# Performance work log

Hardware: AMD Instinct MI355X
Metric: run time of the kernel (lower is better)

The kernel has to match this reference:

```python
import jax, jax.numpy as jnp
import numpy as np

B, DIN, DH, DOUT = 4096, 512, 1024, 256
DFF = 4 * DH
STEPS = 30
REF_DIM = 64
GAMMA = 0.5 * min(1.0, float(np.sqrt(REF_DIM / DIN)))  # dimension-scaled gamma
LN_EPS = 1e-5


def setup_inputs() -> dict:
    key = jax.random.key(0)
    ks = jax.random.split(key, 6)
    rn = lambda k, shp, s: (jax.random.normal(k, shp, jnp.float32) * s)
    return {
        "x": rn(ks[0], (B, DIN), 1.0),
        "embed_w": rn(ks[1], (DH, DIN), 0.02),
        "embed_b": jnp.zeros((DH,), jnp.float32),
        "W1": rn(ks[2], (DFF, DH), 0.02),
        "b1": jnp.zeros((DFF,), jnp.float32),
        "W2": rn(ks[3], (DH, DFF), 0.02),
        "b2": jnp.zeros((DH,), jnp.float32),
        "ln_g": jnp.ones((DH,), jnp.float32),
        "ln_b": jnp.zeros((DH,), jnp.float32),
        "head_w": rn(ks[4], (DOUT, DH), 0.02),
        "head_b": jnp.zeros((DOUT,), jnp.float32),
    }


def _spectral_normalize(W, n_iter=15):
    # power iteration (u, v treated as constants, like torch spectral_norm buffers)
    v0 = jnp.full((W.shape[1],), 1.0 / np.sqrt(W.shape[1]), W.dtype)
    def body(i, uv):
        _, v = uv
        u = W @ v
        u = u / (jnp.linalg.norm(u) + 1e-12)
        v = W.T @ u
        v = v / (jnp.linalg.norm(v) + 1e-12)
        return (u, v)
    u0 = W @ v0
    u0 = u0 / (jnp.linalg.norm(u0) + 1e-12)
    u, v = jax.lax.fori_loop(0, n_iter, body, (u0, v0))
    u = jax.lax.stop_gradient(u)
    v = jax.lax.stop_gradient(v)
    sigma = u @ (W @ v)  # grad flows through W here, as in torch
    return W / sigma


def _layernorm(h, g, b):
    mu = jnp.mean(h, axis=-1, keepdims=True)
    var = jnp.var(h, axis=-1, keepdims=True)
    return (h - mu) * jax.lax.rsqrt(var + LN_EPS) * g + b


def reference(x, embed_w, embed_b, W1, b1, W2, b2, ln_g, ln_b, head_w, head_b):
    W1n = _spectral_normalize(W1)
    W2n = _spectral_normalize(W2)
    x_emb = x @ embed_w.T + embed_b  # [B, DH]; constant across steps

    def ffn(h):
        hn = _layernorm(h, ln_g, ln_b)
        hid = jnp.tanh(hn @ W1n.T + b1)  # dropout p=0 -> identity
        return hid @ W2n.T + b2

    def step(h, _):
        h_target = ffn(h) + x_emb
        h_next = (1.0 - GAMMA) * h + GAMMA * h_target
        return h_next, None

    h, _ = jax.lax.scan(step, x_emb, None, length=STEPS)
    return h @ head_w.T + head_b
```

## Files before the change

kernel.cpp:

```cpp
#include <hip/hip_runtime.h>
#include <hip/hip_bf16.h>
#include <math.h>

#define B_    4096
#define DIN_  512
#define DH_   1024
#define DOUT_ 256
#define DFF_  4096
#define STEPS_ 30
#define GAMMA_ 0.17677669529663687f
#define LN_EPS_ 1e-5f

typedef __attribute__((ext_vector_type(8))) short short8;
typedef __attribute__((ext_vector_type(4))) float f32x4;

__device__ inline void gload_lds16(const void* g, void* l) {
  __builtin_amdgcn_global_load_lds(
      (const __attribute__((address_space(1))) unsigned int*)g,
      (__attribute__((address_space(3))) unsigned int*)l, 16, 0, 0);
}

__device__ inline float fast_tanh(float v) {
  const float e = __expf(2.f * v);
  return 1.f - 2.f * __builtin_amdgcn_rcpf(e + 1.f);
}

__device__ inline float bf2f(unsigned short u) {
  return __uint_as_float((unsigned)u << 16);
}

__global__ __launch_bounds__(512, 2) void gemm256(
    const __hip_bfloat16* __restrict__ A, const __hip_bfloat16* __restrict__ Bm,
    int M, int N, int K, int kc, int nt, const float* __restrict__ bias,
    int epi, __hip_bfloat16* __restrict__ bf16out) {
  __shared__ __align__(16) char lds[4][32768];
  const int tid = threadIdx.x;
  const int lane = tid & 63;
  const int wid = tid >> 6;
  const int wr = wid >> 2;
  const int wc = wid & 3;

  const int gx = gridDim.x;
  const int nwg = gx * gridDim.y;
  const int wg = blockIdx.y * gx + blockIdx.x;
  const int cpx = nwg >> 3;
  const int swz = (wg & 7) * cpx + (wg >> 3);
  const int bx = swz % gx, by = swz / gx;
  const int m0 = by * 256, n0 = bx * 256;
  const int zk = blockIdx.z * kc;

  const int srow = wid * 16 + (lane >> 2);
  const int scol = (lane & 3) * 8;

  f32x4 acc[8][4];
  const f32x4 zero = {0.f, 0.f, 0.f, 0.f};
#pragma unroll
  for (int i = 0; i < 8; ++i)
#pragma unroll
    for (int j = 0; j < 4; ++j) acc[i][j] = zero;

  auto STAGE = [&](int t) {
    const int kt = zk + t * 32;
    char* base = &lds[t & 3][0];
#pragma unroll
    for (int q = 0; q < 4; ++q) {
      const __hip_bfloat16* src =
          (q < 2) ? A + (size_t)(m0 + q * 128 + srow) * K + kt + scol
                  : Bm + (size_t)(n0 + (q - 2) * 128 + srow) * K + kt + scol;
      gload_lds16((const void*)src, (void*)(base + q * 8192 + wid * 1024));
    }
  };

  STAGE(0);
  STAGE(1);
  STAGE(2);

  const int ar = lane & 15;
  const int hb = (lane >> 4) * 16;

  for (int t = 0; t < nt; ++t) {
    const char* base = &lds[t & 3][0];
    if (t + 3 <= nt) {
      asm volatile("s_waitcnt vmcnt(8)" ::: "memory");
    } else if (t + 2 == nt) {
      asm volatile("s_waitcnt vmcnt(4)" ::: "memory");
    } else {
      asm volatile("s_waitcnt vmcnt(0)" ::: "memory");
    }
    __builtin_amdgcn_s_barrier();
    __builtin_amdgcn_sched_barrier(0);

    short8 av[8], bv[4];
#pragma unroll
    for (int mf = 0; mf < 8; ++mf)
      av[mf] = *(const short8*)(base + (wr * 128 + mf * 16 + ar) * 64 + hb);
#pragma unroll
    for (int nf = 0; nf < 4; ++nf)
      bv[nf] = *(const short8*)(base + 16384 + (wc * 64 + nf * 16 + ar) * 64 + hb);

    if (t + 3 < nt) STAGE(t + 3);

    asm volatile("s_waitcnt lgkmcnt(0)" ::: "memory");
    __builtin_amdgcn_sched_barrier(0);
    __builtin_amdgcn_s_setprio(1);
#pragma unroll
    for (int mf = 0; mf < 8; ++mf)
#pragma unroll
      for (int nf = 0; nf < 4; ++nf)
        acc[mf][nf] = __builtin_amdgcn_mfma_f32_16x16x32_bf16(av[mf], bv[nf], acc[mf][nf], 0, 0, 0);
    __builtin_amdgcn_s_setprio(0);
    __builtin_amdgcn_sched_barrier(0);
  }

  if (epi == 4) bf16out += (size_t)blockIdx.z * ((size_t)M * N);
  const int rb = (lane >> 4) * 4;
#pragma unroll
  for (int mf = 0; mf < 8; ++mf) {
#pragma unroll
    for (int nf = 0; nf < 4; ++nf) {
      const int col = n0 + wc * 64 + nf * 16 + ar;
      const float bvs = bias ? bias[col] : 0.f;
#pragma unroll
      for (int j = 0; j < 4; ++j) {
        const int row = m0 + wr * 128 + mf * 16 + rb + j;
        float v = acc[mf][nf][j] + bvs;
        if (epi == 1) v = fast_tanh(v);
        bf16out[(size_t)row * N + col] = __float2bfloat16(v);
      }
    }
  }
}

__global__ __launch_bounds__(256) void gemm_bt(
    const __hip_bfloat16* __restrict__ A, const __hip_bfloat16* __restrict__ Bm,
    int M, int N, int K, const float* __restrict__ bias, int epi,
    float* __restrict__ f32out, float* __restrict__ f32out2) {
  __shared__ __align__(16) short As[128 * 32];
  __shared__ __align__(16) short Bs[128 * 32];
  const int tid = threadIdx.x;
  const int lane = tid & 63;
  const int wid = tid >> 6;
  const int wr = wid >> 1, wc = wid & 1;

  const int gx = gridDim.x;
  const int nwg = gx * gridDim.y;
  const int wg = blockIdx.y * gx + blockIdx.x;
  const int cpx = nwg >> 3;
  const int swz = (wg & 7) * cpx + (wg >> 3);
  const int bx = swz % gx, by = swz / gx;

  const int m0 = by * 128, n0 = bx * 128;
  const int ldsrow = lane >> 2;
  const int col8 = (lane & 3) * 8;

  f32x4 acc[4][4];
  const f32x4 zero = {0.f, 0.f, 0.f, 0.f};
#pragma unroll
  for (int i = 0; i < 4; ++i)
#pragma unroll
    for (int j = 0; j < 4; ++j) acc[i][j] = zero;

  for (int kt = 0; kt < K; kt += 32) {
#pragma unroll
    for (int i = 0; i < 2; ++i) {
      const int seg = wid * 2 + i;
      gload_lds16(A + (size_t)(m0 + seg * 16 + ldsrow) * K + kt + col8,
                  (void*)(As + seg * 512));
      gload_lds16(Bm + (size_t)(n0 + seg * 16 + ldsrow) * K + kt + col8,
                  (void*)(Bs + seg * 512));
    }
    __syncthreads();
    short8 a[4], b[4];
#pragma unroll
    for (int mf = 0; mf < 4; ++mf)
      a[mf] = *(const short8*)&As[(wr * 64 + mf * 16 + (lane & 15)) * 32 + (lane >> 4) * 8];
#pragma unroll
    for (int nf = 0; nf < 4; ++nf)
      b[nf] = *(const short8*)&Bs[(wc * 64 + nf * 16 + (lane & 15)) * 32 + (lane >> 4) * 8];
#pragma unroll
    for (int mf = 0; mf < 4; ++mf)
#pragma unroll
      for (int nf = 0; nf < 4; ++nf)
        acc[mf][nf] = __builtin_amdgcn_mfma_f32_16x16x32_bf16(a[mf], b[nf], acc[mf][nf], 0, 0, 0);
    __syncthreads();
  }

  const int rbase = (lane >> 4) * 4;
  const int cin = lane & 15;
#pragma unroll
  for (int mf = 0; mf < 4; ++mf) {
#pragma unroll
    for (int nf = 0; nf < 4; ++nf) {
      const int col = n0 + wc * 64 + nf * 16 + cin;
      const float bv = bias[col];
#pragma unroll
      for (int j = 0; j < 4; ++j) {
        const int row = m0 + wr * 64 + mf * 16 + rbase + j;
        const float v = acc[mf][nf][j] + bv;
        const size_t idx = (size_t)row * N + col;
        if (epi == 0) {
          f32out[idx] = v;
          f32out2[idx] = v;
        } else {
          f32out[idx] = v;
        }
      }
    }
  }
}

__global__ __launch_bounds__(256) void reduce_ln_kernel(
    const __hip_bfloat16* __restrict__ ps, const float* __restrict__ b2,
    const float* __restrict__ xe, float* __restrict__ h,
    const float* __restrict__ g, const float* __restrict__ be,
    __hip_bfloat16* __restrict__ outbf, int do_ln) {
  const int row = blockIdx.x, tid = threadIdx.x;
  const size_t base = (size_t)row * DH_;
  const size_t slab = (size_t)B_ * DH_;
  float pv0 = 0.f, pv1 = 0.f, pv2 = 0.f, pv3 = 0.f;
#pragma unroll
  for (int z = 0; z < 4; ++z) {
    const ushort4 q = ((const ushort4*)(ps + z * slab + base))[tid];
    pv0 += bf2f(q.x); pv1 += bf2f(q.y); pv2 += bf2f(q.z); pv3 += bf2f(q.w);
  }
  const float4 xv = ((const float4*)(xe + base))[tid];
  const float4 hv = ((const float4*)(h + base))[tid];
  const float4 bv = ((const float4*)b2)[tid];
  float4 nv;
  nv.x = (1.f - GAMMA_) * hv.x + GAMMA_ * (pv0 + bv.x + xv.x);
  nv.y = (1.f - GAMMA_) * hv.y + GAMMA_ * (pv1 + bv.y + xv.y);
  nv.z = (1.f - GAMMA_) * hv.z + GAMMA_ * (pv2 + bv.z + xv.z);
  nv.w = (1.f - GAMMA_) * hv.w + GAMMA_ * (pv3 + bv.w + xv.w);
  ((float4*)(h + base))[tid] = nv;

  __hip_bfloat16* out = outbf + base + tid * 4;
  if (!do_ln) {
    out[0] = __float2bfloat16(nv.x);
    out[1] = __float2bfloat16(nv.y);
    out[2] = __float2bfloat16(nv.z);
    out[3] = __float2bfloat16(nv.w);
    return;
  }
  float s = nv.x + nv.y + nv.z + nv.w;
  float ss = nv.x * nv.x + nv.y * nv.y + nv.z * nv.z + nv.w * nv.w;
#pragma unroll
  for (int o = 32; o > 0; o >>= 1) {
    s += __shfl_down(s, o, 64);
    ss += __shfl_down(ss, o, 64);
  }
  __shared__ float rs_[4], rss_[4];
  const int lane = tid & 63, wid = tid >> 6;
  if (lane == 0) { rs_[wid] = s; rss_[wid] = ss; }
  __syncthreads();
  const float tot = rs_[0] + rs_[1] + rs_[2] + rs_[3];
  const float tots = rss_[0] + rss_[1] + rss_[2] + rss_[3];
  const float mu = tot * (1.f / DH_);
  const float var = tots * (1.f / DH_) - mu * mu;
  const float rstd = rsqrtf(var + LN_EPS_);
  const float4 gv = ((const float4*)g)[tid];
  const float4 bev = ((const float4*)be)[tid];
  out[0] = __float2bfloat16((nv.x - mu) * rstd * gv.x + bev.x);
  out[1] = __float2bfloat16((nv.y - mu) * rstd * gv.y + bev.y);
  out[2] = __float2bfloat16((nv.z - mu) * rstd * gv.z + bev.z);
  out[3] = __float2bfloat16((nv.w - mu) * rstd * gv.w + bev.w);
}

__global__ __launch_bounds__(256) void ln_cast_kernel(
    const float* __restrict__ h, const float* __restrict__ g,
    const float* __restrict__ be, __hip_bfloat16* __restrict__ hn) {
  const int row = blockIdx.x;
  const int tid = threadIdx.x;
  const float4 v = ((const float4*)(h + (size_t)row * DH_))[tid];
  float s = v.x + v.y + v.z + v.w;
  float ss = v.x * v.x + v.y * v.y + v.z * v.z + v.w * v.w;
#pragma unroll
  for (int o = 32; o > 0; o >>= 1) {
    s += __shfl_down(s, o, 64);
    ss += __shfl_down(ss, o, 64);
  }
  __shared__ float rs_[4], rss_[4];
  const int lane = tid & 63, wid = tid >> 6;
  if (lane == 0) { rs_[wid] = s; rss_[wid] = ss; }
  __syncthreads();
  const float tot = rs_[0] + rs_[1] + rs_[2] + rs_[3];
  const float tots = rss_[0] + rss_[1] + rss_[2] + rss_[3];
  const float mu = tot * (1.f / DH_);
  const float var = tots * (1.f / DH_) - mu * mu;
  const float rstd = rsqrtf(var + LN_EPS_);
  const float4 gv = ((const float4*)g)[tid];
  const float4 bv = ((const float4*)be)[tid];
  __hip_bfloat16* out = hn + (size_t)row * DH_ + tid * 4;
  out[0] = __float2bfloat16((v.x - mu) * rstd * gv.x + bv.x);
  out[1] = __float2bfloat16((v.y - mu) * rstd * gv.y + bv.y);
  out[2] = __float2bfloat16((v.z - mu) * rstd * gv.z + bv.z);
  out[3] = __float2bfloat16((v.w - mu) * rstd * gv.w + bv.w);
}

__global__ __launch_bounds__(256) void matvec2_kernel(
    const float* __restrict__ Wa, const float* __restrict__ xa,
    float* __restrict__ ya, int rowsA, int colsA,
    const float* __restrict__ Wb, const float* __restrict__ xb,
    float* __restrict__ yb, int rowsB, int colsB) {
  const int gw = (int)(blockIdx.x * 256 + threadIdx.x) >> 6;
  const int lane = threadIdx.x & 63;
  const float* W;
  const float* x;
  float* y;
  int row, cols;
  if (gw < rowsA) {
    W = Wa; x = xa; y = ya; row = gw; cols = colsA;
  } else {
    row = gw - rowsA;
    if (row >= rowsB) return;
    W = Wb; x = xb; y = yb; cols = colsB;
  }
  const float4* wr = (const float4*)(W + (size_t)row * cols);
  const float4* xv = (const float4*)x;
  const int n4 = cols >> 2;
  float s = 0.f;
  for (int c = lane; c < n4; c += 64) {
    const float4 wv = wr[c];
    const float4 vv = xv[c];
    s += wv.x * vv.x + wv.y * vv.y + wv.z * vv.z + wv.w * vv.w;
  }
#pragma unroll
  for (int o = 32; o > 0; o >>= 1) s += __shfl_down(s, o, 64);
  if (lane == 0) y[row] = s;
}

__global__ __launch_bounds__(256) void transpose_kernel(
    const float* __restrict__ in, float* __restrict__ out, int R, int C) {
  __shared__ float t[32][33];
  const int lx = threadIdx.x & 31, ly = threadIdx.x >> 5;
  const int r0 = blockIdx.y * 32, c0 = blockIdx.x * 32;
#pragma unroll
  for (int j = 0; j < 32; j += 8) t[ly + j][lx] = in[(size_t)(r0 + ly + j) * C + c0 + lx];
  __syncthreads();
#pragma unroll
  for (int j = 0; j < 32; j += 8) out[(size_t)(c0 + ly + j) * R + r0 + lx] = t[lx][ly + j];
}

__global__ void init_v_kernel(float* v1, float* v2) {
  const int i = blockIdx.x * 256 + threadIdx.x;
  if (i < 1024) v1[i] = 0.03125f;
  if (i < 4096) v2[i] = 0.015625f;
}

__global__ __launch_bounds__(256) void cast_kernel(
    const float* __restrict__ s, __hip_bfloat16* __restrict__ d, int n) {
  const int b = (blockIdx.x * 256 + threadIdx.x) * 4;
  if (b < n) {
    const float4 v = *(const float4*)(s + b);
    d[b] = __float2bfloat16(v.x);
    d[b + 1] = __float2bfloat16(v.y);
    d[b + 2] = __float2bfloat16(v.z);
    d[b + 3] = __float2bfloat16(v.w);
  }
}

__global__ __launch_bounds__(256) void cast_scaled_kernel(
    const float* __restrict__ s, __hip_bfloat16* __restrict__ d, int n,
    const float* __restrict__ rs) {
  const float r = rs[0];
  const int b = (blockIdx.x * 256 + threadIdx.x) * 4;
  if (b < n) {
    const float4 v = *(const float4*)(s + b);
    d[b] = __float2bfloat16(v.x * r);
    d[b + 1] = __float2bfloat16(v.y * r);
    d[b + 2] = __float2bfloat16(v.z * r);
    d[b + 3] = __float2bfloat16(v.w * r);
  }
}

__global__ __launch_bounds__(256) void sigma_rs_kernel(
    const float* __restrict__ c, int m, const float* __restrict__ dv, int n,
    float* __restrict__ rs) {
  const int tid = threadIdx.x;
  float sc = 0.f, sd = 0.f;
  for (int i = tid; i < m; i += 256) { const float v = c[i]; sc += v * v; }
  for (int i = tid; i < n; i += 256) { const float v = dv[i]; sd += v * v; }
#pragma unroll
  for (int o = 32; o > 0; o >>= 1) {
    sc += __shfl_down(sc, o, 64);
    sd += __shfl_down(sd, o, 64);
  }
  __shared__ float a[4], b[4];
  const int lane = tid & 63, wid = tid >> 6;
  if (lane == 0) { a[wid] = sc; b[wid] = sd; }
  __syncthreads();
  if (tid == 0) {
    const float tc = a[0] + a[1] + a[2] + a[3];
    const float td = b[0] + b[1] + b[2] + b[3];
    rs[0] = sqrtf(tc / td);
  }
}

extern "C" void kernel_launch(void* const* d_in, const int* in_sizes, int n_in,
                              void* d_out, int out_size, void* d_ws, size_t ws_size,
                              hipStream_t stream) {
  const float* x       = (const float*)d_in[0];
  const float* embed_w = (const float*)d_in[1];
  const float* embed_b = (const float*)d_in[2];
  const float* W1      = (const float*)d_in[3];
  const float* b1      = (const float*)d_in[4];
  const float* W2      = (const float*)d_in[5];
  const float* b2      = (const float*)d_in[6];
  const float* ln_g    = (const float*)d_in[7];
  const float* ln_b    = (const float*)d_in[8];
  const float* head_w  = (const float*)d_in[9];
  const float* head_b  = (const float*)d_in[10];
  float* out = (float*)d_out;

  char* p = (char*)d_ws;
  auto carve = [&](size_t bytes) {
    char* r = p;
    p += (bytes + 255) & ~(size_t)255;
    return (void*)r;
  };
  float* h     = (float*)carve((size_t)B_ * DH_ * 4);
  float* x_emb = (float*)carve((size_t)B_ * DH_ * 4);
  float* W1T   = (float*)carve((size_t)DFF_ * DH_ * 4);
  float* W2T   = (float*)carve((size_t)DH_ * DFF_ * 4);
  __hip_bfloat16* ps = (__hip_bfloat16*)W1T;
  __hip_bfloat16* hn   = (__hip_bfloat16*)carve((size_t)B_ * DH_ * 2);
  __hip_bfloat16* hid  = (__hip_bfloat16*)carve((size_t)B_ * DFF_ * 2);
  __hip_bfloat16* W1n  = (__hip_bfloat16*)carve((size_t)DFF_ * DH_ * 2);
  __hip_bfloat16* W2n  = (__hip_bfloat16*)carve((size_t)DH_ * DFF_ * 2);
  __hip_bfloat16* xbf  = (__hip_bfloat16*)carve((size_t)B_ * DIN_ * 2);
  __hip_bfloat16* ewbf = (__hip_bfloat16*)carve((size_t)DH_ * DIN_ * 2);
  __hip_bfloat16* hwbf = (__hip_bfloat16*)carve((size_t)DOUT_ * DH_ * 2);
  __hip_bfloat16* hbf  = (__hip_bfloat16*)carve((size_t)B_ * DH_ * 2);
  float* v1a = (float*)carve(4096 * 4);
  float* v1b = (float*)carve(4096 * 4);
  float* c1  = (float*)carve(4096 * 4);
  float* v2a = (float*)carve(4096 * 4);
  float* v2b = (float*)carve(4096 * 4);
  float* c2  = (float*)carve(4096 * 4);
  float* rs1 = (float*)carve(256);
  float* rs2 = (float*)carve(256);

  transpose_kernel<<<dim3(DH_ / 32, DFF_ / 32), 256, 0, stream>>>(W1, W1T, DFF_, DH_);
  transpose_kernel<<<dim3(DFF_ / 32, DH_ / 32), 256, 0, stream>>>(W2, W2T, DH_, DFF_);
  init_v_kernel<<<16, 256, 0, stream>>>(v1a, v2a);
  cast_kernel<<<(B_ * DIN_ / 4) / 256, 256, 0, stream>>>(x, xbf, B_ * DIN_);
  cast_kernel<<<(DH_ * DIN_ / 4) / 256, 256, 0, stream>>>(embed_w, ewbf, DH_ * DIN_);
  cast_kernel<<<(DOUT_ * DH_ / 4) / 256, 256, 0, stream>>>(head_w, hwbf, DOUT_ * DH_);

  gemm_bt<<<dim3(DH_ / 128, B_ / 128), 256, 0, stream>>>(
      xbf, ewbf, B_, DH_, DIN_, embed_b, 0, x_emb, h);

  for (int it = 0; it < 15; ++it) {
    const float* vin1 = (it & 1) ? v1b : v1a;
    float* vout1 = (it & 1) ? v1a : v1b;
    const float* vin2 = (it & 1) ? v2b : v2a;
    float* vout2 = (it & 1) ? v2a : v2b;
    matvec2_kernel<<<((DFF_ + DH_) * 64) / 256, 256, 0, stream>>>(
        W1, vin1, c1, DFF_, DH_, W2, vin2, c2, DH_, DFF_);
    matvec2_kernel<<<((DH_ + DFF_) * 64) / 256, 256, 0, stream>>>(
        W1T, c1, vout1, DH_, DFF_, W2T, c2, vout2, DFF_, DH_);
  }
  sigma_rs_kernel<<<1, 256, 0, stream>>>(c1, DFF_, v1b, DH_, rs1);
  sigma_rs_kernel<<<1, 256, 0, stream>>>(c2, DH_, v2b, DFF_, rs2);
  cast_scaled_kernel<<<(DFF_ * DH_ / 4) / 256, 256, 0, stream>>>(W1, W1n, DFF_ * DH_, rs1);
  cast_scaled_kernel<<<(DH_ * DFF_ / 4) / 256, 256, 0, stream>>>(W2, W2n, DH_ * DFF_, rs2);

  ln_cast_kernel<<<B_, 256, 0, stream>>>(h, ln_g, ln_b, hn);

  for (int s = 0; s < STEPS_; ++s) {
    gemm256<<<dim3(DFF_ / 256, B_ / 256, 1), 512, 0, stream>>>(
        hn, W1n, B_, DFF_, DH_, DH_, DH_ / 32, b1, 1, hid);
    gemm256<<<dim3(DH_ / 256, B_ / 256, 4), 512, 0, stream>>>(
        hid, W2n, B_, DH_, DFF_, DFF_ / 4, DFF_ / 4 / 32, nullptr, 4, ps);
    const int last = (s == STEPS_ - 1);
    reduce_ln_kernel<<<B_, 256, 0, stream>>>(
        ps, b2, x_emb, h, ln_g, ln_b, last ? hbf : hn, last ? 0 : 1);
  }

  gemm_bt<<<dim3(DOUT_ / 128, B_ / 128), 256, 0, stream>>>(
      hbf, hwbf, B_, DOUT_, DH_, head_b, 3, out, nullptr);
}
```

Before: 3.340 ms.

## Restructure gemm256 to BK=64 double-buffered LDS with XOR swizzle and split fragment loads

The main 256x256 GEMM tile now uses a K-step of 64 instead of 32, with two LDS buffers instead of four. Tiles are stored with an XOR-swizzled column layout to avoid LDS bank conflicts on the 128-byte rows. The fragment loads are split into four quarter phases interleaved with MFMA groups to cut register pressure, and a trailing barrier guards buffer reuse. The aim is fewer barriers per K and conflict-free LDS reads. In exchange, prefetch depth drops from three stages to one-ahead double buffering.

```diff
diff --git a/kernel.cpp b/kernel.cpp
--- a/kernel.cpp
+++ b/kernel.cpp
@@ -33,7 +33,7 @@
     const __hip_bfloat16* __restrict__ A, const __hip_bfloat16* __restrict__ Bm,
     int M, int N, int K, int kc, int nt, const float* __restrict__ bias,
     int epi, __hip_bfloat16* __restrict__ bf16out) {
-  __shared__ __align__(16) char lds[4][32768];
+  __shared__ __align__(16) char lds[131072];
   const int tid = threadIdx.x;
   const int lane = tid & 63;
   const int wid = tid >> 6;
@@ -49,8 +49,8 @@
   const int m0 = by * 256, n0 = bx * 256;
   const int zk = blockIdx.z * kc;
 
-  const int srow = wid * 16 + (lane >> 2);
-  const int scol = (lane & 3) * 8;
+  const int scol = ((lane & 7) ^ (lane >> 3)) * 8;
+  const int srow = lane >> 3;
 
   f32x4 acc[8][4];
   const f32x4 zero = {0.f, 0.f, 0.f, 0.f};
@@ -60,60 +60,116 @@
     for (int j = 0; j < 4; ++j) acc[i][j] = zero;
 
   auto STAGE = [&](int t) {
-    const int kt = zk + t * 32;
-    char* base = &lds[t & 3][0];
-#pragma unroll
-    for (int q = 0; q < 4; ++q) {
-      const __hip_bfloat16* src =
-          (q < 2) ? A + (size_t)(m0 + q * 128 + srow) * K + kt + scol
-                  : Bm + (size_t)(n0 + (q - 2) * 128 + srow) * K + kt + scol;
-      gload_lds16((const void*)src, (void*)(base + q * 8192 + wid * 1024));
+    const int kt = zk + t * 64;
+    char* ab = &lds[(t & 1) * 32768];
+    char* bb = &lds[65536 + (t & 1) * 32768];
+#pragma unroll
+    for (int i = 0; i < 4; ++i) {
+      const int rbase = wid * 32 + i * 8;
+      const int r = rbase + srow;
+      gload_lds16(A + (size_t)(m0 + r) * K + kt + scol, ab + rbase * 128);
+      gload_lds16(Bm + (size_t)(n0 + r) * K + kt + scol, bb + rbase * 128);
     }
   };
 
   STAGE(0);
   STAGE(1);
-  STAGE(2);
 
   const int ar = lane & 15;
-  const int hb = (lane >> 4) * 16;
+  const int hi = lane >> 4;
+  const int a7 = ar & 7;
+  const int co0 = ((0 * 4 + hi) ^ a7) * 16;
+  const int co1 = ((1 * 4 + hi) ^ a7) * 16;
 
   for (int t = 0; t < nt; ++t) {
-    const char* base = &lds[t & 3][0];
-    if (t + 3 <= nt) {
+    const int buf = t & 1;
+    const char* Ab = &lds[buf * 32768];
+    const char* Bb = &lds[65536 + buf * 32768];
+    const int arow = (wr * 128 + ar) * 128;
+    const int brow = (wc * 64 + ar) * 128;
+
+    if (t == nt - 1) {
+      asm volatile("s_waitcnt vmcnt(0)" ::: "memory");
+    } else {
       asm volatile("s_waitcnt vmcnt(8)" ::: "memory");
-    } else if (t + 2 == nt) {
-      asm volatile("s_waitcnt vmcnt(4)" ::: "memory");
-    } else {
-      asm volatile("s_waitcnt vmcnt(0)" ::: "memory");
     }
     __builtin_amdgcn_s_barrier();
     __builtin_amdgcn_sched_barrier(0);
 
-    short8 av[8], bv[4];
-#pragma unroll
-    for (int mf = 0; mf < 8; ++mf)
-      av[mf] = *(const short8*)(base + (wr * 128 + mf * 16 + ar) * 64 + hb);
-#pragma unroll
-    for (int nf = 0; nf < 4; ++nf)
-      bv[nf] = *(const short8*)(base + 16384 + (wc * 64 + nf * 16 + ar) * 64 + hb);
-
-    if (t + 3 < nt) STAGE(t + 3);
-
+    short8 a[4][2], b[4][2];
+#pragma unroll
+    for (int i = 0; i < 4; ++i) {
+      a[i][0] = *(const short8*)(Ab + arow + i * 2048 + co0);
+      a[i][1] = *(const short8*)(Ab + arow + i * 2048 + co1);
+    }
+#pragma unroll
+    for (int j = 0; j < 2; ++j) {
+      b[j][0] = *(const short8*)(Bb + brow + j * 2048 + co0);
+      b[j][1] = *(const short8*)(Bb + brow + j * 2048 + co1);
+    }
     asm volatile("s_waitcnt lgkmcnt(0)" ::: "memory");
     __builtin_amdgcn_sched_barrier(0);
     __builtin_amdgcn_s_setprio(1);
 #pragma unroll
-    for (int mf = 0; mf < 8; ++mf)
-#pragma unroll
-      for (int nf = 0; nf < 4; ++nf)
-        acc[mf][nf] = __builtin_amdgcn_mfma_f32_16x16x32_bf16(av[mf], bv[nf], acc[mf][nf], 0, 0, 0);
+    for (int i = 0; i < 4; ++i)
+#pragma unroll
+      for (int j = 0; j < 2; ++j)
+#pragma unroll
+        for (int ks = 0; ks < 2; ++ks)
+          acc[i][j] = __builtin_amdgcn_mfma_f32_16x16x32_bf16(a[i][ks], b[j][ks], acc[i][j], 0, 0, 0);
     __builtin_amdgcn_s_setprio(0);
     __builtin_amdgcn_sched_barrier(0);
+#pragma unroll
+    for (int j = 0; j < 2; ++j) {
+      b[2 + j][0] = *(const short8*)(Bb + brow + (2 + j) * 2048 + co0);
+      b[2 + j][1] = *(const short8*)(Bb + brow + (2 + j) * 2048 + co1);
+    }
+    asm volatile("s_waitcnt lgkmcnt(0)" ::: "memory");
+    __builtin_amdgcn_sched_barrier(0);
+    __builtin_amdgcn_s_setprio(1);
+#pragma unroll
+    for (int i = 0; i < 4; ++i)
+#pragma unroll
+      for (int j = 0; j < 2; ++j)
+#pragma unroll
+        for (int ks = 0; ks < 2; ++ks)
+          acc[i][2 + j] = __builtin_amdgcn_mfma_f32_16x16x32_bf16(a[i][ks], b[2 + j][ks], acc[i][2 + j], 0, 0, 0);
+    __builtin_amdgcn_s_setprio(0);
+    __builtin_amdgcn_sched_barrier(0);
+#pragma unroll
+    for (int i = 0; i < 4; ++i) {
+      a[i][0] = *(const short8*)(Ab + arow + (4 + i) * 2048 + co0);
+      a[i][1] = *(const short8*)(Ab + arow + (4 + i) * 2048 + co1);
+    }
+    asm volatile("s_waitcnt lgkmcnt(0)" ::: "memory");
+    __builtin_amdgcn_sched_barrier(0);
+    __builtin_amdgcn_s_setprio(1);
+#pragma unroll
+    for (int i = 0; i < 4; ++i)
+#pragma unroll
+      for (int j = 0; j < 2; ++j)
+#pragma unroll
+        for (int ks = 0; ks < 2; ++ks)
+          acc[4 + i][2 + j] = __builtin_amdgcn_mfma_f32_16x16x32_bf16(a[i][ks], b[2 + j][ks], acc[4 + i][2 + j], 0, 0, 0);
+    __builtin_amdgcn_s_setprio(0);
+    __builtin_amdgcn_sched_barrier(0);
+    __builtin_amdgcn_s_setprio(1);
+#pragma unroll
+    for (int i = 0; i < 4; ++i)
+#pragma unroll
+      for (int j = 0; j < 2; ++j)
+#pragma unroll
+        for (int ks = 0; ks < 2; ++ks)
+          acc[4 + i][j] = __builtin_amdgcn_mfma_f32_16x16x32_bf16(a[i][ks], b[j][ks], acc[4 + i][j], 0, 0, 0);
+    __builtin_amdgcn_s_setprio(0);
+    __builtin_amdgcn_sched_barrier(0);
+    __builtin_amdgcn_s_barrier();
+    __builtin_amdgcn_sched_barrier(0);
+    if (t + 2 < nt) STAGE(t + 2);
   }
 
   if (epi == 4) bf16out += (size_t)blockIdx.z * ((size_t)M * N);
-  const int rb = (lane >> 4) * 4;
+  const int rb = hi * 4;
 #pragma unroll
   for (int mf = 0; mf < 8; ++mf) {
 #pragma unroll
@@ -468,9 +524,9 @@
 
   for (int s = 0; s < STEPS_; ++s) {
     gemm256<<<dim3(DFF_ / 256, B_ / 256, 1), 512, 0, stream>>>(
-        hn, W1n, B_, DFF_, DH_, DH_, DH_ / 32, b1, 1, hid);
+        hn, W1n, B_, DFF_, DH_, DH_, DH_ / 64, b1, 1, hid);
     gemm256<<<dim3(DH_ / 256, B_ / 256, 4), 512, 0, stream>>>(
-        hid, W2n, B_, DH_, DFF_, DFF_ / 4, DFF_ / 4 / 32, nullptr, 4, ps);
+        hid, W2n, B_, DH_, DFF_, DFF_ / 4, DFF_ / 4 / 64, nullptr, 4, ps);
     const int last = (s == STEPS_ - 1);
     reduce_ln_kernel<<<B_, 256, 0, stream>>>(
         ps, b2, x_emb, h, ln_g, ln_b, last ? hbf : hn, last ? 0 : 1);
```

Result: no change. 3.327 ms (-0.4%).
